# Kernel optimization log

Measured on AMD Instinct MI355X. Metric: run time of the kernel, lower is better.

Reference implementation:

```python
import jax, jax.numpy as jnp
import numpy as np

BN_EPS = 1e-5


def gcn_layer(x, src, dst, n, W, b):
    loop = jnp.arange(n)
    s = jnp.concatenate([src, loop])
    d = jnp.concatenate([dst, loop])
    deg = jax.ops.segment_sum(jnp.ones_like(s, dtype=x.dtype), d, num_segments=n)
    dinv = jnp.where(deg > 0, deg ** -0.5, 0.0)
    norm = dinv[s] * dinv[d]                      # [E+N]
    h = x @ W                                     # [N, out]
    msg = h[s] * norm[:, None]                    # gather + scale
    agg = jax.ops.segment_sum(msg, d, num_segments=n)
    return agg + b


def batchnorm(x, gamma, beta):
    # training-mode BN over the node dimension (biased variance, as in torch)
    m = jnp.mean(x, axis=0)
    v = jnp.var(x, axis=0)
    return (x - m) * jax.lax.rsqrt(v + BN_EPS) * gamma + beta


def setup_inputs() -> dict:
    key = jax.random.key(0)
    ks = jax.random.split(key, 4)
    N, E, D = 50000, 800000, 128
    x = jax.random.normal(ks[0], (N, D), dtype=jnp.float32)
    edge_index = jax.random.randint(ks[1], (2, E), 0, N, dtype=jnp.int64)
    W1 = jax.random.normal(ks[2], (D, D), dtype=jnp.float32) * (1.0 / np.sqrt(D))
    W2 = jax.random.normal(ks[3], (D, D), dtype=jnp.float32) * (1.0 / np.sqrt(D))
    return {
        "x": x, "edge_index": edge_index,
        "W1": W1, "b1": jnp.zeros((D,), jnp.float32),
        "gamma1": jnp.ones((D,), jnp.float32), "beta1": jnp.zeros((D,), jnp.float32),
        "W2": W2, "b2": jnp.zeros((D,), jnp.float32),
        "gamma2": jnp.ones((D,), jnp.float32), "beta2": jnp.zeros((D,), jnp.float32),
    }


def reference(x, edge_index, W1, b1, gamma1, beta1, W2, b2, gamma2, beta2):
    n = x.shape[0]
    src, dst = edge_index[0], edge_index[1]
    h = gcn_layer(x, src, dst, n, W1, b1)
    h = jax.nn.relu(batchnorm(h, gamma1, beta1))
    # dropout is identity in deterministic reference
    h = gcn_layer(h, src, dst, n, W2, b2)
    h = jax.nn.relu(batchnorm(h, gamma2, beta2))
    return h
```

## Files before the change

kernel.cpp:

```cpp
#include <hip/hip_runtime.h>

static constexpr float BN_EPS = 1e-5f;
#define ELLW 64
#define STATB 512

typedef short short8 __attribute__((ext_vector_type(8)));
typedef float f32x4 __attribute__((ext_vector_type(4)));
union BF8 { short8 v; unsigned u[4]; uint4 q; };

__device__ __forceinline__ unsigned rne_bf16(float f) {
    unsigned u = __float_as_uint(f);
    u += 0x7fffu + ((u >> 16) & 1u);
    return u >> 16;
}
__device__ __forceinline__ float bflo(unsigned u) { return __uint_as_float(u << 16); }
__device__ __forceinline__ float bfhi(unsigned u) { return __uint_as_float(u & 0xffff0000u); }

__global__ __launch_bounds__(256) void k_detect_i64(const unsigned* __restrict__ ei,
                                                    int* __restrict__ flag) {
    if (blockIdx.x == 0 && threadIdx.x == 0) {
        int allz = 1;
        for (int i = 0; i < 256; ++i) {
            if (ei[2 * i + 1] != 0u) { allz = 0; break; }
        }
        *flag = allz;
    }
}

__global__ __launch_bounds__(256) void k_ell(const void* __restrict__ eidx, int E,
                                             const int* __restrict__ flag,
                                             int* __restrict__ deg,
                                             int* __restrict__ rec,
                                             int2* __restrict__ ovf,
                                             int* __restrict__ ovf_cnt, int ovf_cap) {
    const int base = blockIdx.x * 1024 + threadIdx.x;
    const bool is64 = (*flag != 0);
    int s[4], d[4];
    bool ok[4];
#pragma unroll
    for (int j = 0; j < 4; ++j) {
        int e = base + j * 256;
        ok[j] = e < E;
        if (ok[j]) {
            if (is64) {
                s[j] = (int)((const long long*)eidx)[e];
                d[j] = (int)((const long long*)eidx)[E + e];
            } else {
                s[j] = ((const int*)eidx)[e];
                d[j] = ((const int*)eidx)[E + e];
            }
        }
    }
    int pos[4];
#pragma unroll
    for (int j = 0; j < 4; ++j)
        if (ok[j]) pos[j] = atomicAdd(&deg[d[j]], 1);
#pragma unroll
    for (int j = 0; j < 4; ++j) {
        if (!ok[j]) continue;
        if (pos[j] < ELLW) {
            rec[(size_t)d[j] * ELLW + pos[j]] = s[j];
        } else {
            int o = atomicAdd(ovf_cnt, 1);
            if (o < ovf_cap) ovf[o] = make_int2(s[j], d[j]);
        }
    }
}

__global__ __launch_bounds__(256) void k_gemm_mfma(const float* __restrict__ X,
                                                   const float* __restrict__ W,
                                                   int n,
                                                   const float* __restrict__ scale,
                                                   const float* __restrict__ shift,
                                                   unsigned short* __restrict__ Yb,
                                                   float* __restrict__ Yf) {
    __shared__ unsigned short Xh[64][136];
    __shared__ unsigned short Xl[64][136];
    const int tid = threadIdx.x;
    const int lane = tid & 63;
    const int w = tid >> 6;
    const int row0 = blockIdx.x * 64;
    const int kb = (lane >> 4) * 8;
    const int cl16 = lane & 15;

    BF8 Bh[4][2], Bl[4][2];
#pragma unroll
    for (int ks = 0; ks < 4; ++ks) {
#pragma unroll
        for (int nn = 0; nn < 2; ++nn) {
            const float* wp = W + (size_t)(ks * 32 + kb) * 128 + w * 32 + nn * 16 + cl16;
            unsigned uh[8], ul[8];
#pragma unroll
            for (int j = 0; j < 8; ++j) {
                float v = wp[(size_t)j * 128];
                unsigned h = rne_bf16(v);
                unsigned l = rne_bf16(v - __uint_as_float(h << 16));
                uh[j] = h; ul[j] = l;
            }
#pragma unroll
            for (int t = 0; t < 4; ++t) {
                Bh[ks][nn].u[t] = uh[2 * t] | (uh[2 * t + 1] << 16);
                Bl[ks][nn].u[t] = ul[2 * t] | (ul[2 * t + 1] << 16);
            }
        }
    }

    for (int i = tid; i < 64 * 32; i += 256) {
        int r = i >> 5, c = i & 31;
        int gr = row0 + r;
        float4 v = (gr < n) ? ((const float4*)X)[(size_t)gr * 32 + c]
                            : float4{0.f, 0.f, 0.f, 0.f};
        if (scale) {
            float4 sc = ((const float4*)scale)[c];
            float4 sh = ((const float4*)shift)[c];
            v.x = fmaxf(fmaf(v.x, sc.x, sh.x), 0.f);
            v.y = fmaxf(fmaf(v.y, sc.y, sh.y), 0.f);
            v.z = fmaxf(fmaf(v.z, sc.z, sh.z), 0.f);
            v.w = fmaxf(fmaf(v.w, sc.w, sh.w), 0.f);
        }
#pragma unroll
        for (int j = 0; j < 4; ++j) {
            float f = (&v.x)[j];
            unsigned h = rne_bf16(f);
            unsigned l = rne_bf16(f - __uint_as_float(h << 16));
            Xh[r][c * 4 + j] = (unsigned short)h;
            Xl[r][c * 4 + j] = (unsigned short)l;
        }
    }
    __syncthreads();

    f32x4 acc[4][2];
#pragma unroll
    for (int m = 0; m < 4; ++m)
#pragma unroll
        for (int nn = 0; nn < 2; ++nn) acc[m][nn] = f32x4{0.f, 0.f, 0.f, 0.f};
#pragma unroll
    for (int ks = 0; ks < 4; ++ks) {
        BF8 Ah[4], Al[4];
#pragma unroll
        for (int m = 0; m < 4; ++m) {
            const int r = m * 16 + cl16;
            const int cc = ks * 32 + kb;
            Ah[m].q = *(const uint4*)&Xh[r][cc];
            Al[m].q = *(const uint4*)&Xl[r][cc];
        }
#pragma unroll
        for (int m = 0; m < 4; ++m) {
#pragma unroll
            for (int nn = 0; nn < 2; ++nn) {
                acc[m][nn] = __builtin_amdgcn_mfma_f32_16x16x32_bf16(Ah[m].v, Bh[ks][nn].v, acc[m][nn], 0, 0, 0);
                acc[m][nn] = __builtin_amdgcn_mfma_f32_16x16x32_bf16(Ah[m].v, Bl[ks][nn].v, acc[m][nn], 0, 0, 0);
                acc[m][nn] = __builtin_amdgcn_mfma_f32_16x16x32_bf16(Al[m].v, Bh[ks][nn].v, acc[m][nn], 0, 0, 0);
            }
        }
    }

    const int rb2 = (lane >> 4) * 4;
#pragma unroll
    for (int m = 0; m < 4; ++m) {
#pragma unroll
        for (int nn = 0; nn < 2; ++nn) {
            const int col = w * 32 + nn * 16 + cl16;
#pragma unroll
            for (int r = 0; r < 4; ++r) {
                int gr = row0 + m * 16 + rb2 + r;
                if (gr < n) {
                    float val = acc[m][nn][r];
                    if (Yb) Yb[(size_t)gr * 128 + col] = (unsigned short)rne_bf16(val);
                    if (Yf) Yf[(size_t)gr * 128 + col] = val;
                }
            }
        }
    }
}

__global__ __launch_bounds__(256) void k_gemm_f32(const float* __restrict__ X,
                                                  const float* __restrict__ W,
                                                  int n,
                                                  float* __restrict__ Yf) {
    __shared__ float Ws[128 * 128];
    __shared__ float Xs[32 * 128];
    const int tid = threadIdx.x;
    for (int i = tid; i < 128 * 32; i += 256)
        ((float4*)Ws)[i] = ((const float4*)W)[i];
    const int row0 = blockIdx.x * 32;
    for (int i = tid; i < 32 * 32; i += 256) {
        int r = i >> 5, c = i & 31;
        int gr = row0 + r;
        float4 v = (gr < n) ? ((const float4*)X)[(size_t)gr * 32 + c]
                            : float4{0.f, 0.f, 0.f, 0.f};
        ((float4*)Xs)[i] = v;
    }
    __syncthreads();
    const int c4 = (tid & 31) * 4;
    const int rb = tid >> 5;
    float4 acc[4];
#pragma unroll
    for (int j = 0; j < 4; ++j) acc[j] = float4{0.f, 0.f, 0.f, 0.f};
    for (int k = 0; k < 128; ++k) {
        float4 w = *(const float4*)&Ws[k * 128 + c4];
#pragma unroll
        for (int j = 0; j < 4; ++j) {
            float xv = Xs[(rb + 8 * j) * 128 + k];
            acc[j].x = fmaf(xv, w.x, acc[j].x);
            acc[j].y = fmaf(xv, w.y, acc[j].y);
            acc[j].z = fmaf(xv, w.z, acc[j].z);
            acc[j].w = fmaf(xv, w.w, acc[j].w);
        }
    }
#pragma unroll
    for (int j = 0; j < 4; ++j) {
        int r = row0 + rb + 8 * j;
        if (r < n) *(float4*)&Yf[(size_t)r * 128 + c4] = acc[j];
    }
}

__global__ __launch_bounds__(256) void k_agg(const int* __restrict__ rec,
                                             const int* __restrict__ deg,
                                             const unsigned* __restrict__ Hb,
                                             const float* __restrict__ bias,
                                             float* __restrict__ B, int n) {
    const int d = blockIdx.x * 4 + (threadIdx.x >> 6);
    if (d >= n) return;
    const int lane = threadIdx.x & 63;
    const int cnt = __builtin_amdgcn_readfirstlane(deg[d]);
    const int cl = cnt < ELLW ? cnt : ELLW;
    const float dinv_d = rsqrtf((float)(cnt + 1));
    const float selfn = dinv_d * dinv_d;
    unsigned hu = Hb[(size_t)d * 64 + lane];
    float2 bb = ((const float2*)bias)[lane];
    float accx = fmaf(bflo(hu), selfn, bb.x);
    float accy = fmaf(bfhi(hu), selfn, bb.y);
    const int* row = rec + (size_t)d * ELLW;
    int e = 0;
    for (; e + 3 < cl; e += 4) {
        int4 ra = *(const int4*)&row[e];
        float n0 = rsqrtf((float)(deg[ra.x] + 1)) * dinv_d;
        float n1 = rsqrtf((float)(deg[ra.y] + 1)) * dinv_d;
        float n2 = rsqrtf((float)(deg[ra.z] + 1)) * dinv_d;
        float n3 = rsqrtf((float)(deg[ra.w] + 1)) * dinv_d;
        unsigned u0 = Hb[(size_t)ra.x * 64 + lane];
        unsigned u1 = Hb[(size_t)ra.y * 64 + lane];
        unsigned u2 = Hb[(size_t)ra.z * 64 + lane];
        unsigned u3 = Hb[(size_t)ra.w * 64 + lane];
        accx = fmaf(bflo(u0), n0, accx); accy = fmaf(bfhi(u0), n0, accy);
        accx = fmaf(bflo(u1), n1, accx); accy = fmaf(bfhi(u1), n1, accy);
        accx = fmaf(bflo(u2), n2, accx); accy = fmaf(bfhi(u2), n2, accy);
        accx = fmaf(bflo(u3), n3, accx); accy = fmaf(bfhi(u3), n3, accy);
    }
    for (; e < cl; ++e) {
        int r = row[e];
        float n0 = rsqrtf((float)(deg[r] + 1)) * dinv_d;
        unsigned u0 = Hb[(size_t)r * 64 + lane];
        accx = fmaf(bflo(u0), n0, accx); accy = fmaf(bfhi(u0), n0, accy);
    }
    ((float2*)(B + (size_t)d * 128))[lane] = make_float2(accx, accy);
}

__global__ __launch_bounds__(256) void k_ovf(const int2* __restrict__ ovf,
                                             const int* __restrict__ ovf_cnt,
                                             const int* __restrict__ deg,
                                             const unsigned* __restrict__ Hb,
                                             float* __restrict__ B, int ovf_cap) {
    int m = *ovf_cnt;
    if (m > ovf_cap) m = ovf_cap;
    const int lane = threadIdx.x & 63;
    for (int i = blockIdx.x * 4 + (threadIdx.x >> 6); i < m; i += gridDim.x * 4) {
        int2 sd = ovf[i];
        float nrm = rsqrtf((float)(deg[sd.x] + 1)) * rsqrtf((float)(deg[sd.y] + 1));
        unsigned u = Hb[(size_t)sd.x * 64 + lane];
        atomicAdd(&B[(size_t)sd.y * 128 + 2 * lane], bflo(u) * nrm);
        atomicAdd(&B[(size_t)sd.y * 128 + 2 * lane + 1], bfhi(u) * nrm);
    }
}

__global__ __launch_bounds__(256) void k_bnstats(const float* __restrict__ B, int n,
                                                 float* __restrict__ partials) {
    __shared__ float rs[256], rss[256];
    int col = threadIdx.x & 127;
    int rg = threadIdx.x >> 7;
    float s = 0.f, ss = 0.f;
    for (int r = blockIdx.x * 2 + rg; r < n; r += gridDim.x * 2) {
        float v = B[(size_t)r * 128 + col];
        s += v;
        ss = fmaf(v, v, ss);
    }
    rs[threadIdx.x] = s;
    rss[threadIdx.x] = ss;
    __syncthreads();
    if (threadIdx.x < 128) {
        partials[blockIdx.x * 256 + threadIdx.x] = rs[threadIdx.x] + rs[threadIdx.x + 128];
        partials[blockIdx.x * 256 + 128 + threadIdx.x] = rss[threadIdx.x] + rss[threadIdx.x + 128];
    }
}

__global__ __launch_bounds__(1024) void k_bnfold(const float* __restrict__ partials,
                                                 const float* __restrict__ gamma,
                                                 const float* __restrict__ beta,
                                                 float invn, int nblk,
                                                 float* __restrict__ scale,
                                                 float* __restrict__ shift) {
    __shared__ float ls[8][128], lq[8][128];
    const int col = threadIdx.x & 127;
    const int grp = threadIdx.x >> 7;
    float s = 0.f, ss = 0.f;
#pragma unroll 4
    for (int b = grp; b < nblk; b += 8) {
        s += partials[b * 256 + col];
        ss += partials[b * 256 + 128 + col];
    }
    ls[grp][col] = s;
    lq[grp][col] = ss;
    __syncthreads();
    if (threadIdx.x < 128) {
        int c = threadIdx.x;
        float st = 0.f, sq = 0.f;
#pragma unroll
        for (int g = 0; g < 8; ++g) { st += ls[g][c]; sq += lq[g][c]; }
        float m = st * invn;
        float var = fmaf(-m, m, sq * invn);
        float sc = rsqrtf(var + BN_EPS) * gamma[c];
        scale[c] = sc;
        shift[c] = fmaf(-m, sc, beta[c]);
    }
}

__global__ __launch_bounds__(256) void k_bnapply(const float* __restrict__ Bin,
                                                 float* __restrict__ out,
                                                 const float* __restrict__ scale,
                                                 const float* __restrict__ shift,
                                                 int n) {
    int idx = blockIdx.x * 256 + threadIdx.x;
    if (idx >= n * 32) return;
    int c4 = idx & 31;
    float4 x = ((const float4*)Bin)[idx];
    float4 sc = ((const float4*)scale)[c4];
    float4 sh = ((const float4*)shift)[c4];
    float4 o;
    o.x = fmaxf(fmaf(x.x, sc.x, sh.x), 0.f);
    o.y = fmaxf(fmaf(x.y, sc.y, sh.y), 0.f);
    o.z = fmaxf(fmaf(x.z, sc.z, sh.z), 0.f);
    o.w = fmaxf(fmaf(x.w, sc.w, sh.w), 0.f);
    ((float4*)out)[idx] = o;
}

__global__ __launch_bounds__(256) void k_init_deg(int* __restrict__ deg, int n) {
    int i = blockIdx.x * 256 + threadIdx.x;
    if (i < n) deg[i] = 1;
}

__global__ __launch_bounds__(256) void k_count_deg(const void* __restrict__ eidx, int E,
                                                   const int* __restrict__ flag,
                                                   int* __restrict__ deg) {
    int e = blockIdx.x * 256 + threadIdx.x;
    if (e >= E) return;
    int d;
    if (*flag) d = (int)((const long long*)eidx)[E + e];
    else       d = ((const int*)eidx)[E + e];
    atomicAdd(&deg[d], 1);
}

__global__ __launch_bounds__(256) void k_dinv(const int* __restrict__ deg,
                                              float* __restrict__ dinv, int n) {
    int i = blockIdx.x * 256 + threadIdx.x;
    if (i < n) dinv[i] = rsqrtf((float)deg[i]);
}

__global__ __launch_bounds__(256) void k_selfloop(const float* __restrict__ H,
                                                  const float* __restrict__ dinv,
                                                  const float* __restrict__ bias,
                                                  float* __restrict__ B, int n) {
    int idx = blockIdx.x * 256 + threadIdx.x;
    if (idx >= n * 32) return;
    int r = idx >> 5, c = idx & 31;
    float s = dinv[r];
    s *= s;
    float4 h = ((const float4*)H)[idx];
    float4 bb = ((const float4*)bias)[c];
    float4 o{fmaf(h.x, s, bb.x), fmaf(h.y, s, bb.y),
             fmaf(h.z, s, bb.z), fmaf(h.w, s, bb.w)};
    ((float4*)B)[idx] = o;
}

__global__ __launch_bounds__(256) void k_edge(const void* __restrict__ eidx, int E,
                                              const int* __restrict__ flag,
                                              const float* __restrict__ dinv,
                                              const float* __restrict__ H,
                                              float* __restrict__ B) {
    int e = blockIdx.x * 8 + (threadIdx.x >> 5);
    if (e >= E) return;
    int lane = threadIdx.x & 31;
    int s, d;
    if (*flag) {
        s = (int)((const long long*)eidx)[e];
        d = (int)((const long long*)eidx)[E + e];
    } else {
        s = ((const int*)eidx)[e];
        d = ((const int*)eidx)[E + e];
    }
    float nrm = dinv[s] * dinv[d];
    float4 h = ((const float4*)(H + (size_t)s * 128))[lane];
    float* out = B + (size_t)d * 128 + lane * 4;
    atomicAdd(out + 0, h.x * nrm);
    atomicAdd(out + 1, h.y * nrm);
    atomicAdd(out + 2, h.z * nrm);
    atomicAdd(out + 3, h.w * nrm);
}

static inline char* align256(char* p) {
    return (char*)(((uintptr_t)p + 255) & ~(uintptr_t)255);
}

extern "C" void kernel_launch(void* const* d_in, const int* in_sizes, int n_in,
                              void* d_out, int out_size, void* d_ws, size_t ws_size,
                              hipStream_t stream) {
    const float* x   = (const float*)d_in[0];
    const void*  ei  = d_in[1];
    const float* W1  = (const float*)d_in[2];
    const float* b1  = (const float*)d_in[3];
    const float* g1  = (const float*)d_in[4];
    const float* be1 = (const float*)d_in[5];
    const float* W2  = (const float*)d_in[6];
    const float* b2  = (const float*)d_in[7];
    const float* g2  = (const float*)d_in[8];
    const float* be2 = (const float*)d_in[9];

    const int n = in_sizes[0] / 128;
    const int E = in_sizes[1] / 2;
    const float invn = 1.0f / (float)n;
    float* out = (float*)d_out;

    const int nb_n   = (n + 255) / 256;
    const int nb_e   = (E + 255) / 256;
    const int nb_e4  = (E + 1023) / 1024;
    const int nb_el  = (n * 32 + 255) / 256;
    const int nb_gm  = (n + 63) / 64;
    const int nb_gf  = (n + 31) / 32;
    const int nb_edge = (E + 7) / 8;
    const int nb_agg = (n + 3) / 4;

    char* p = (char*)d_ws;
    float* B = (float*)p;                      p += (size_t)n * 128 * 4;
    unsigned short* Ab = (unsigned short*)p;   p += (size_t)n * 128 * 2;
    p = align256(p);
    int* rec = (int*)p;                        p += (size_t)n * ELLW * 4;
    int2* ovf = (int2*)p;                      p += (size_t)E * 8;
    int* deg = (int*)p;                        p += (size_t)n * 4;
    int* ovf_cnt = (int*)p;                    p += 4;
    p = align256(p);
    float* partials = (float*)p;               p += (size_t)STATB * 256 * 4;
    float* scale = (float*)p;                  p += 128 * 4;
    float* shift = (float*)p;                  p += 128 * 4;
    int* flag = (int*)p;                       p += 16;
    const bool ell_ok = (size_t)(p - (char*)d_ws) <= ws_size;

    if (ell_ok) {
        k_detect_i64<<<1, 256, 0, stream>>>((const unsigned*)ei, flag);
        hipMemsetAsync(deg, 0, (size_t)n * 4 + 4, stream);
        k_ell<<<nb_e4, 256, 0, stream>>>(ei, E, flag, deg, rec, ovf, ovf_cnt, E);

        k_gemm_mfma<<<nb_gm, 256, 0, stream>>>(x, W1, n, nullptr, nullptr, Ab, nullptr);
        k_agg<<<nb_agg, 256, 0, stream>>>(rec, deg, (const unsigned*)Ab, b1, B, n);
        k_ovf<<<64, 256, 0, stream>>>(ovf, ovf_cnt, deg, (const unsigned*)Ab, B, E);
        k_bnstats<<<STATB, 256, 0, stream>>>(B, n, partials);
        k_bnfold<<<1, 1024, 0, stream>>>(partials, g1, be1, invn, STATB, scale, shift);

        k_gemm_mfma<<<nb_gm, 256, 0, stream>>>(B, W2, n, scale, shift, Ab, nullptr);
        k_agg<<<nb_agg, 256, 0, stream>>>(rec, deg, (const unsigned*)Ab, b2, B, n);
        k_ovf<<<64, 256, 0, stream>>>(ovf, ovf_cnt, deg, (const unsigned*)Ab, B, E);
        k_bnstats<<<STATB, 256, 0, stream>>>(B, n, partials);
        k_bnfold<<<1, 1024, 0, stream>>>(partials, g2, be2, invn, STATB, scale, shift);
        k_bnapply<<<nb_el, 256, 0, stream>>>(B, out, scale, shift, n);
    } else {
        char* q = (char*)d_ws;
        float* A = (float*)q;        q += (size_t)n * 128 * 4;
        float* Bf = (float*)q;       q += (size_t)n * 128 * 4;
        int* degf = (int*)q;         q += (size_t)n * 4;
        float* dinv = (float*)q;     q += (size_t)n * 4;
        q = align256(q);
        float* part = (float*)q;     q += (size_t)STATB * 256 * 4;
        float* sc = (float*)q;       q += 128 * 4;
        float* sh = (float*)q;       q += 128 * 4;
        int* flg = (int*)q;          q += 16;

        k_detect_i64<<<1, 256, 0, stream>>>((const unsigned*)ei, flg);
        k_init_deg<<<nb_n, 256, 0, stream>>>(degf, n);
        k_count_deg<<<nb_e, 256, 0, stream>>>(ei, E, flg, degf);
        k_dinv<<<nb_n, 256, 0, stream>>>(degf, dinv, n);

        k_gemm_f32<<<nb_gf, 256, 0, stream>>>(x, W1, n, A);
        k_selfloop<<<nb_el, 256, 0, stream>>>(A, dinv, b1, Bf, n);
        k_edge<<<nb_edge, 256, 0, stream>>>(ei, E, flg, dinv, A, Bf);
        k_bnstats<<<STATB, 256, 0, stream>>>(Bf, n, part);
        k_bnfold<<<1, 1024, 0, stream>>>(part, g1, be1, invn, STATB, sc, sh);
        k_bnapply<<<nb_el, 256, 0, stream>>>(Bf, Bf, sc, sh, n);

        k_gemm_f32<<<nb_gf, 256, 0, stream>>>(Bf, W2, n, A);
        k_selfloop<<<nb_el, 256, 0, stream>>>(A, dinv, b2, Bf, n);
        k_edge<<<nb_edge, 256, 0, stream>>>(ei, E, flg, dinv, A, Bf);
        k_bnstats<<<STATB, 256, 0, stream>>>(Bf, n, part);
        k_bnfold<<<1, 1024, 0, stream>>>(part, g2, be2, invn, STATB, sc, sh);
        k_bnapply<<<nb_el, 256, 0, stream>>>(Bf, out, sc, sh, n);
    }
}
```

Before: 229.4 us.

## Pack source index and fp16 source norm into ELL entries for aggregation

Adds a pass after ELL construction that packs each neighbour's source index (upper 16 bits) together with its fp16 dinv (lower 16 bits) into the same int slot. Aggregation kernels then read the norm straight from the ELL row, which removes the dependent random gather of deg[src] and its rsqrt, and the main loop is unrolled to 8 edges so more row gathers are in flight. The cost is an extra kernel launch and fp16 rounding of the norms, and the path is only enabled when n < 65536.

```diff
diff --git a/kernel.cpp b/kernel.cpp
--- a/kernel.cpp
+++ b/kernel.cpp
@@ -1,4 +1,5 @@
 #include <hip/hip_runtime.h>
+#include <hip/hip_fp16.h>
 
 static constexpr float BN_EPS = 1e-5f;
 #define ELLW 64
@@ -64,6 +65,22 @@
             int o = atomicAdd(ovf_cnt, 1);
             if (o < ovf_cap) ovf[o] = make_int2(s[j], d[j]);
         }
+    }
+}
+
+__global__ __launch_bounds__(256) void k_pack(int* __restrict__ rec,
+                                              const int* __restrict__ deg, int n) {
+    const int d = blockIdx.x * 4 + (threadIdx.x >> 6);
+    if (d >= n) return;
+    const int lane = threadIdx.x & 63;
+    const int cnt = __builtin_amdgcn_readfirstlane(deg[d]);
+    const int cl = cnt < ELLW ? cnt : ELLW;
+    if (lane < cl) {
+        int* p = rec + (size_t)d * ELLW + lane;
+        unsigned s = (unsigned)*p;
+        float ds = rsqrtf((float)(deg[s] + 1));
+        unsigned h = __half_as_ushort(__float2half(ds));
+        *p = (int)((s << 16) | h);
     }
 }
 
@@ -215,6 +232,7 @@
     }
 }
 
+template <bool PACKED>
 __global__ __launch_bounds__(256) void k_agg(const int* __restrict__ rec,
                                              const int* __restrict__ deg,
                                              const unsigned* __restrict__ Hb,
@@ -233,26 +251,68 @@
     float accy = fmaf(bfhi(hu), selfn, bb.y);
     const int* row = rec + (size_t)d * ELLW;
     int e = 0;
-    for (; e + 3 < cl; e += 4) {
-        int4 ra = *(const int4*)&row[e];
-        float n0 = rsqrtf((float)(deg[ra.x] + 1)) * dinv_d;
-        float n1 = rsqrtf((float)(deg[ra.y] + 1)) * dinv_d;
-        float n2 = rsqrtf((float)(deg[ra.z] + 1)) * dinv_d;
-        float n3 = rsqrtf((float)(deg[ra.w] + 1)) * dinv_d;
-        unsigned u0 = Hb[(size_t)ra.x * 64 + lane];
-        unsigned u1 = Hb[(size_t)ra.y * 64 + lane];
-        unsigned u2 = Hb[(size_t)ra.z * 64 + lane];
-        unsigned u3 = Hb[(size_t)ra.w * 64 + lane];
-        accx = fmaf(bflo(u0), n0, accx); accy = fmaf(bfhi(u0), n0, accy);
-        accx = fmaf(bflo(u1), n1, accx); accy = fmaf(bfhi(u1), n1, accy);
-        accx = fmaf(bflo(u2), n2, accx); accy = fmaf(bfhi(u2), n2, accy);
-        accx = fmaf(bflo(u3), n3, accx); accy = fmaf(bfhi(u3), n3, accy);
-    }
-    for (; e < cl; ++e) {
-        int r = row[e];
-        float n0 = rsqrtf((float)(deg[r] + 1)) * dinv_d;
-        unsigned u0 = Hb[(size_t)r * 64 + lane];
-        accx = fmaf(bflo(u0), n0, accx); accy = fmaf(bfhi(u0), n0, accy);
+    if (PACKED) {
+        for (; e + 7 < cl; e += 8) {
+            int4 ra = *(const int4*)&row[e];
+            int4 rb = *(const int4*)&row[e + 4];
+            unsigned s0 = (unsigned)ra.x >> 16, s1 = (unsigned)ra.y >> 16;
+            unsigned s2 = (unsigned)ra.z >> 16, s3 = (unsigned)ra.w >> 16;
+            unsigned s4 = (unsigned)rb.x >> 16, s5 = (unsigned)rb.y >> 16;
+            unsigned s6 = (unsigned)rb.z >> 16, s7 = (unsigned)rb.w >> 16;
+            unsigned u0 = Hb[(size_t)s0 * 64 + lane];
+            unsigned u1 = Hb[(size_t)s1 * 64 + lane];
+            unsigned u2 = Hb[(size_t)s2 * 64 + lane];
+            unsigned u3 = Hb[(size_t)s3 * 64 + lane];
+            unsigned u4 = Hb[(size_t)s4 * 64 + lane];
+            unsigned u5 = Hb[(size_t)s5 * 64 + lane];
+            unsigned u6 = Hb[(size_t)s6 * 64 + lane];
+            unsigned u7 = Hb[(size_t)s7 * 64 + lane];
+            float n0 = __half2float(__ushort_as_half((unsigned short)(ra.x & 0xffff))) * dinv_d;
+            float n1 = __half2float(__ushort_as_half((unsigned short)(ra.y & 0xffff))) * dinv_d;
+            float n2 = __half2float(__ushort_as_half((unsigned short)(ra.z & 0xffff))) * dinv_d;
+            float n3 = __half2float(__ushort_as_half((unsigned short)(ra.w & 0xffff))) * dinv_d;
+            float n4 = __half2float(__ushort_as_half((unsigned short)(rb.x & 0xffff))) * dinv_d;
+            float n5 = __half2float(__ushort_as_half((unsigned short)(rb.y & 0xffff))) * dinv_d;
+            float n6 = __half2float(__ushort_as_half((unsigned short)(rb.z & 0xffff))) * dinv_d;
+            float n7 = __half2float(__ushort_as_half((unsigned short)(rb.w & 0xffff))) * dinv_d;
+            accx = fmaf(bflo(u0), n0, accx); accy = fmaf(bfhi(u0), n0, accy);
+            accx = fmaf(bflo(u1), n1, accx); accy = fmaf(bfhi(u1), n1, accy);
+            accx = fmaf(bflo(u2), n2, accx); accy = fmaf(bfhi(u2), n2, accy);
+            accx = fmaf(bflo(u3), n3, accx); accy = fmaf(bfhi(u3), n3, accy);
+            accx = fmaf(bflo(u4), n4, accx); accy = fmaf(bfhi(u4), n4, accy);
+            accx = fmaf(bflo(u5), n5, accx); accy = fmaf(bfhi(u5), n5, accy);
+            accx = fmaf(bflo(u6), n6, accx); accy = fmaf(bfhi(u6), n6, accy);
+            accx = fmaf(bflo(u7), n7, accx); accy = fmaf(bfhi(u7), n7, accy);
+        }
+        for (; e < cl; ++e) {
+            int r = row[e];
+            unsigned s0 = (unsigned)r >> 16;
+            unsigned u0 = Hb[(size_t)s0 * 64 + lane];
+            float n0 = __half2float(__ushort_as_half((unsigned short)(r & 0xffff))) * dinv_d;
+            accx = fmaf(bflo(u0), n0, accx); accy = fmaf(bfhi(u0), n0, accy);
+        }
+    } else {
+        for (; e + 3 < cl; e += 4) {
+            int4 ra = *(const int4*)&row[e];
+            float n0 = rsqrtf((float)(deg[ra.x] + 1)) * dinv_d;
+            float n1 = rsqrtf((float)(deg[ra.y] + 1)) * dinv_d;
+            float n2 = rsqrtf((float)(deg[ra.z] + 1)) * dinv_d;
+            float n3 = rsqrtf((float)(deg[ra.w] + 1)) * dinv_d;
+            unsigned u0 = Hb[(size_t)ra.x * 64 + lane];
+            unsigned u1 = Hb[(size_t)ra.y * 64 + lane];
+            unsigned u2 = Hb[(size_t)ra.z * 64 + lane];
+            unsigned u3 = Hb[(size_t)ra.w * 64 + lane];
+            accx = fmaf(bflo(u0), n0, accx); accy = fmaf(bfhi(u0), n0, accy);
+            accx = fmaf(bflo(u1), n1, accx); accy = fmaf(bfhi(u1), n1, accy);
+            accx = fmaf(bflo(u2), n2, accx); accy = fmaf(bfhi(u2), n2, accy);
+            accx = fmaf(bflo(u3), n3, accx); accy = fmaf(bfhi(u3), n3, accy);
+        }
+        for (; e < cl; ++e) {
+            int r = row[e];
+            float n0 = rsqrtf((float)(deg[r] + 1)) * dinv_d;
+            unsigned u0 = Hb[(size_t)r * 64 + lane];
+            accx = fmaf(bflo(u0), n0, accx); accy = fmaf(bfhi(u0), n0, accy);
+        }
     }
     ((float2*)(B + (size_t)d * 128))[lane] = make_float2(accx, accy);
 }
@@ -453,20 +513,28 @@
     float* shift = (float*)p;                  p += 128 * 4;
     int* flag = (int*)p;                       p += 16;
     const bool ell_ok = (size_t)(p - (char*)d_ws) <= ws_size;
+    const bool packed = n < 65536;
 
     if (ell_ok) {
         k_detect_i64<<<1, 256, 0, stream>>>((const unsigned*)ei, flag);
         hipMemsetAsync(deg, 0, (size_t)n * 4 + 4, stream);
         k_ell<<<nb_e4, 256, 0, stream>>>(ei, E, flag, deg, rec, ovf, ovf_cnt, E);
+        if (packed) k_pack<<<nb_agg, 256, 0, stream>>>(rec, deg, n);
 
         k_gemm_mfma<<<nb_gm, 256, 0, stream>>>(x, W1, n, nullptr, nullptr, Ab, nullptr);
-        k_agg<<<nb_agg, 256, 0, stream>>>(rec, deg, (const unsigned*)Ab, b1, B, n);
+        if (packed)
+            k_agg<true><<<nb_agg, 256, 0, stream>>>(rec, deg, (const unsigned*)Ab, b1, B, n);
+        else
+            k_agg<false><<<nb_agg, 256, 0, stream>>>(rec, deg, (const unsigned*)Ab, b1, B, n);
         k_ovf<<<64, 256, 0, stream>>>(ovf, ovf_cnt, deg, (const unsigned*)Ab, B, E);
         k_bnstats<<<STATB, 256, 0, stream>>>(B, n, partials);
         k_bnfold<<<1, 1024, 0, stream>>>(partials, g1, be1, invn, STATB, scale, shift);
 
         k_gemm_mfma<<<nb_gm, 256, 0, stream>>>(B, W2, n, scale, shift, Ab, nullptr);
-        k_agg<<<nb_agg, 256, 0, stream>>>(rec, deg, (const unsigned*)Ab, b2, B, n);
+        if (packed)
+            k_agg<true><<<nb_agg, 256, 0, stream>>>(rec, deg, (const unsigned*)Ab, b2, B, n);
+        else
+            k_agg<false><<<nb_agg, 256, 0, stream>>>(rec, deg, (const unsigned*)Ab, b2, B, n);
         k_ovf<<<64, 256, 0, stream>>>(ovf, ovf_cnt, deg, (const unsigned*)Ab, B, E);
         k_bnstats<<<STATB, 256, 0, stream>>>(B, n, partials);
         k_bnfold<<<1, 1024, 0, stream>>>(partials, g2, be2, invn, STATB, scale, shift);
```

Measured after the change: 236.3 us. 3.0% more time.

## Build ELL adjacency via two-pass bucketing by destination group

Applied to the files above, without the earlier changes.

Replaces the single-pass ELL construction, which scattered atomics and writes randomly across all nodes, with two passes. The first pass appends edges into buckets of 16 destinations with packed src/dst-low bits. A per-bucket kernel then fills the ELL rows, so atomics and writes stay within a small, cache-local region. Buckets that overflow fall back to the old direct path. It adds an extra kernel launch, an intermediate buffer pass, and a larger workspace, and the packed encoding limits the src range (s<<4 must fit in 32 bits).

```diff
diff --git a/kernel.cpp b/kernel.cpp
--- a/kernel.cpp
+++ b/kernel.cpp
@@ -3,6 +3,8 @@
 static constexpr float BN_EPS = 1e-5f;
 #define ELLW 64
 #define STATB 512
+#define BSHIFT 4
+#define BCAP 320
 
 typedef short short8 __attribute__((ext_vector_type(8)));
 typedef float f32x4 __attribute__((ext_vector_type(4)));
@@ -27,12 +29,14 @@
     }
 }
 
-__global__ __launch_bounds__(256) void k_ell(const void* __restrict__ eidx, int E,
-                                             const int* __restrict__ flag,
-                                             int* __restrict__ deg,
-                                             int* __restrict__ rec,
-                                             int2* __restrict__ ovf,
-                                             int* __restrict__ ovf_cnt, int ovf_cap) {
+__global__ __launch_bounds__(256) void k_bucket(const void* __restrict__ eidx, int E,
+                                                const int* __restrict__ flag,
+                                                int* __restrict__ bcnt,
+                                                int* __restrict__ bbuf,
+                                                int* __restrict__ deg,
+                                                int* __restrict__ rec,
+                                                int2* __restrict__ ovf,
+                                                int* __restrict__ ovf_cnt, int ovf_cap) {
     const int base = blockIdx.x * 1024 + threadIdx.x;
     const bool is64 = (*flag != 0);
     int s[4], d[4];
@@ -54,15 +58,45 @@
     int pos[4];
 #pragma unroll
     for (int j = 0; j < 4; ++j)
-        if (ok[j]) pos[j] = atomicAdd(&deg[d[j]], 1);
+        if (ok[j]) pos[j] = atomicAdd(&bcnt[d[j] >> BSHIFT], 1);
 #pragma unroll
     for (int j = 0; j < 4; ++j) {
         if (!ok[j]) continue;
-        if (pos[j] < ELLW) {
-            rec[(size_t)d[j] * ELLW + pos[j]] = s[j];
+        if (pos[j] < BCAP) {
+            bbuf[(size_t)(d[j] >> BSHIFT) * BCAP + pos[j]] =
+                (s[j] << BSHIFT) | (d[j] & ((1 << BSHIFT) - 1));
+        } else {
+            int p2 = atomicAdd(&deg[d[j]], 1);
+            if (p2 < ELLW) {
+                rec[(size_t)d[j] * ELLW + p2] = s[j];
+            } else {
+                int o = atomicAdd(ovf_cnt, 1);
+                if (o < ovf_cap) ovf[o] = make_int2(s[j], d[j]);
+            }
+        }
+    }
+}
+
+__global__ __launch_bounds__(256) void k_fill(const int* __restrict__ bcnt,
+                                              const int* __restrict__ bbuf,
+                                              int* __restrict__ deg,
+                                              int* __restrict__ rec,
+                                              int2* __restrict__ ovf,
+                                              int* __restrict__ ovf_cnt, int ovf_cap) {
+    const int b = blockIdx.x;
+    const int d0 = b << BSHIFT;
+    int m = bcnt[b];
+    if (m > BCAP) m = BCAP;
+    for (int i = threadIdx.x; i < m; i += 256) {
+        unsigned r = (unsigned)bbuf[(size_t)b * BCAP + i];
+        int s = (int)(r >> BSHIFT);
+        int d = d0 | (int)(r & ((1u << BSHIFT) - 1u));
+        int pos = atomicAdd(&deg[d], 1);
+        if (pos < ELLW) {
+            rec[(size_t)d * ELLW + pos] = s;
         } else {
             int o = atomicAdd(ovf_cnt, 1);
-            if (o < ovf_cap) ovf[o] = make_int2(s[j], d[j]);
+            if (o < ovf_cap) ovf[o] = make_int2(s, d);
         }
     }
 }
@@ -438,6 +472,7 @@
     const int nb_gf  = (n + 31) / 32;
     const int nb_edge = (E + 7) / 8;
     const int nb_agg = (n + 3) / 4;
+    const int nbkt   = (n + (1 << BSHIFT) - 1) >> BSHIFT;
 
     char* p = (char*)d_ws;
     float* B = (float*)p;                      p += (size_t)n * 128 * 4;
@@ -445,8 +480,10 @@
     p = align256(p);
     int* rec = (int*)p;                        p += (size_t)n * ELLW * 4;
     int2* ovf = (int2*)p;                      p += (size_t)E * 8;
+    int* bbuf = (int*)p;                       p += (size_t)nbkt * BCAP * 4;
     int* deg = (int*)p;                        p += (size_t)n * 4;
     int* ovf_cnt = (int*)p;                    p += 4;
+    int* bcnt = (int*)p;                       p += (size_t)nbkt * 4;
     p = align256(p);
     float* partials = (float*)p;               p += (size_t)STATB * 256 * 4;
     float* scale = (float*)p;                  p += 128 * 4;
@@ -456,8 +493,9 @@
 
     if (ell_ok) {
         k_detect_i64<<<1, 256, 0, stream>>>((const unsigned*)ei, flag);
-        hipMemsetAsync(deg, 0, (size_t)n * 4 + 4, stream);
-        k_ell<<<nb_e4, 256, 0, stream>>>(ei, E, flag, deg, rec, ovf, ovf_cnt, E);
+        hipMemsetAsync(deg, 0, (size_t)n * 4 + 4 + (size_t)nbkt * 4, stream);
+        k_bucket<<<nb_e4, 256, 0, stream>>>(ei, E, flag, bcnt, bbuf, deg, rec, ovf, ovf_cnt, E);
+        k_fill<<<nbkt, 256, 0, stream>>>(bcnt, bbuf, deg, rec, ovf, ovf_cnt, E);
 
         k_gemm_mfma<<<nb_gm, 256, 0, stream>>>(x, W1, n, nullptr, nullptr, Ab, nullptr);
         k_agg<<<nb_agg, 256, 0, stream>>>(rec, deg, (const unsigned*)Ab, b1, B, n);
```

Measured after the change: 283.3 us. 23.5% more time.
